# Kernel optimization log

Hardware: AMD Instinct MI355X
Metric: run time of the kernel (lower is better)

## Reference

```python
import jax, jax.numpy as jnp
import numpy as np

N_ATOMS = 50000
N_BONDS = 100000
MAX_NB = 6
ATOM_FDIM = 133
BOND_FDIM = 147
HIDDEN = 512
DEPTH = 5
N_MOLS = 2048


def setup_inputs() -> dict:
    key = jax.random.key(0)
    ks = jax.random.split(key, 10)
    f_atoms = jax.random.normal(ks[0], (N_ATOMS, ATOM_FDIM), dtype=jnp.float32)
    f_bonds = jax.random.normal(ks[1], (N_BONDS, BOND_FDIM), dtype=jnp.float32)
    a2b = jax.random.randint(ks[2], (N_ATOMS, MAX_NB), 0, N_BONDS, dtype=jnp.int32)
    b2a = jax.random.randint(ks[3], (N_BONDS,), 0, N_ATOMS, dtype=jnp.int32)
    # reverse bond of directed bond i is its pair i^1 (chemprop layout)
    b2revb = (jnp.arange(N_BONDS, dtype=jnp.int32) ^ 1)
    mol_ids = jnp.sort(jax.random.randint(ks[4], (N_ATOMS,), 0, N_MOLS, dtype=jnp.int32))
    W_i = jax.random.normal(ks[5], (BOND_FDIM, HIDDEN), dtype=jnp.float32) * 0.05
    W_h = jax.random.normal(ks[6], (HIDDEN, HIDDEN), dtype=jnp.float32) * 0.05
    W_o = jax.random.normal(ks[7], (ATOM_FDIM + HIDDEN, HIDDEN), dtype=jnp.float32) * 0.05
    b_o = jnp.zeros((HIDDEN,), dtype=jnp.float32)
    return {"f_atoms": f_atoms, "f_bonds": f_bonds, "a2b": a2b, "b2a": b2a,
            "b2revb": b2revb, "mol_ids": mol_ids, "W_i": W_i, "W_h": W_h,
            "W_o": W_o, "b_o": b_o, "n_mols": N_MOLS}


def _dmpnn_forward(f_atoms, f_bonds, a2b, b2a, b2revb, mol_ids,
                   W_i, W_h, W_o, b_o, n_mols):
    # input = W_i(f_bonds); message = act(input)   (bond messages, bias=False)
    inp = f_bonds @ W_i                      # [n_bonds, H]
    message = jax.nn.relu(inp)
    for _ in range(DEPTH - 1):
        nei = message[a2b]                   # gather: [n_atoms, max_nb, H]
        a_message = nei.sum(axis=1)          # [n_atoms, H]
        rev_message = message[b2revb]        # [n_bonds, H]
        message = a_message[b2a] - rev_message
        message = jax.nn.relu(inp + message @ W_h)
    # final atom aggregation
    nei = message[a2b]                       # [n_atoms, max_nb, H]
    a_message = nei.sum(axis=1)              # [n_atoms, H]
    a_input = jnp.concatenate([f_atoms, a_message], axis=1)
    atom_hiddens = jax.nn.relu(a_input @ W_o + b_o)   # [n_atoms, H]
    # scope-based mean aggregation per molecule (== a_scope loop, mean)
    sums = jax.ops.segment_sum(atom_hiddens, mol_ids, num_segments=n_mols)
    counts = jax.ops.segment_sum(jnp.ones((atom_hiddens.shape[0],), atom_hiddens.dtype),
                                 mol_ids, num_segments=n_mols)
    mol_vecs = jnp.where(counts[:, None] > 0, sums / jnp.maximum(counts, 1.0)[:, None], 0.0)
    return mol_vecs


def reference(f_atoms, f_bonds, a2b, b2a, b2revb, mol_ids, W_i, W_h, W_o, b_o, n_mols):
    return _dmpnn_forward(f_atoms, f_bonds, a2b, b2a, b2revb, mol_ids,
                          W_i, W_h, W_o, b_o, n_mols)
```

## Files before the change

### kernel.cpp

```cpp
#include <hip/hip_runtime.h>

typedef unsigned int u32;
typedef unsigned short u16;

constexpr int N_ATOMS   = 50000;
constexpr int N_BONDS   = 100000;
constexpr int MAX_NB    = 6;
constexpr int ATOM_FDIM = 133;
constexpr int BOND_FDIM = 147;
constexpr int HIDDEN    = 512;
constexpr int DEPTH     = 5;
constexpr int N_MOLS    = 2048;
constexpr int KB_PAD    = 160;
constexpr int KC        = 672;

typedef short bf16x8 __attribute__((ext_vector_type(8)));
typedef float f32x4  __attribute__((ext_vector_type(4)));

__device__ __forceinline__ float b2f(u32 u) {
    u <<= 16; float f; __builtin_memcpy(&f, &u, 4); return f;
}
__device__ __forceinline__ u16 f2b(float f) {
    u32 u; __builtin_memcpy(&u, &f, 4);
    u = (u + 0x7fffu + ((u >> 16) & 1u)) >> 16;
    return (u16)u;
}
__device__ __forceinline__ u32 pack2(float x, float y) {
    return (u32)f2b(x) | ((u32)f2b(y) << 16);
}
__device__ __forceinline__ float load_in(const void* p, size_t i, u32 bf) {
    return bf ? b2f((u32)((const u16*)p)[i]) : ((const float*)p)[i];
}

__global__ void k_detect(const void* fb, u32* flag) {
    if (threadIdx.x == 0 && blockIdx.x == 0) {
        const u16* p = (const u16*)fb;
        int cnt = 0;
        for (int i = 0; i < 64; ++i) {
            const u32 e = (p[i] >> 7) & 0xFF;
            if (e >= 110 && e <= 140) ++cnt;
        }
        *flag = (cnt >= 52) ? 1u : 0u;
    }
}

template <int SPLIT, int MODE>
__global__ void gemm_bt(const u16* __restrict__ A, int ldaA,
                        const u16* __restrict__ A2,
                        const u16* __restrict__ BT, int ldb,
                        const u16* __restrict__ bias,
                        u16* __restrict__ out,
                        int M, int K)
{
    __shared__ u16 As[128 * 32];
    __shared__ u16 Bs[128 * 32];
    const int t    = threadIdx.x;
    const int w    = t >> 6;
    const int l    = t & 63;
    const int quad = l >> 4;
    const int lr   = l & 15;
    const int bm0  = blockIdx.x * 128;
    const int bn0  = blockIdx.y * 128;
    const int wr   = (w >> 1) * 64;
    const int wc   = (w & 1) * 64;

    f32x4 acc[4][4];
#pragma unroll
    for (int i = 0; i < 4; ++i)
#pragma unroll
        for (int j = 0; j < 4; ++j) acc[i][j] = (f32x4){0.f, 0.f, 0.f, 0.f};

    const int kt_n = K >> 5;
    for (int kt = 0; kt < kt_n; ++kt) {
        const int k0 = kt << 5;
        const u16* srcA;
        int lda, kcol;
        if (SPLIT && kt >= 5) { srcA = A2; lda = HIDDEN; kcol = k0 - KB_PAD; }
        else                  { srcA = A;  lda = ldaA;   kcol = k0; }
        __syncthreads();
#pragma unroll
        for (int p = 0; p < 2; ++p) {
            const int c  = p * 256 + t;
            const int r  = c >> 2;
            const int kg = c & 3;
            int rowA = bm0 + r; if (rowA >= M) rowA = M - 1;
            const uint4 va = *(const uint4*)(srcA + (size_t)rowA * lda + kcol + kg * 8);
            const int rowB = bn0 + r;
            const uint4 vb = *(const uint4*)(BT + (size_t)rowB * ldb + k0 + kg * 8);
            *(uint4*)(As + c * 8) = va;
            *(uint4*)(Bs + c * 8) = vb;
        }
        __syncthreads();

        bf16x8 af[4], bfr[4];
#pragma unroll
        for (int i = 0; i < 4; ++i) {
            af[i]  = *(const bf16x8*)(As + (wr + i * 16 + lr) * 32 + quad * 8);
            bfr[i] = *(const bf16x8*)(Bs + (wc + i * 16 + lr) * 32 + quad * 8);
        }
#pragma unroll
        for (int i = 0; i < 4; ++i)
#pragma unroll
            for (int j = 0; j < 4; ++j)
                acc[i][j] = __builtin_amdgcn_mfma_f32_16x16x32_bf16(
                    af[i], bfr[j], acc[i][j], 0, 0, 0);
    }

#pragma unroll
    for (int i = 0; i < 4; ++i) {
        const int row0 = bm0 + wr + i * 16 + quad * 4;
#pragma unroll
        for (int j = 0; j < 4; ++j) {
            const int col = bn0 + wc + j * 16 + lr;
#pragma unroll
            for (int r = 0; r < 4; ++r) {
                const int row = row0 + r;
                if (row < M) {
                    float v = acc[i][j][r];
                    if (MODE == 1) v += b2f((u32)bias[col]);
                    out[(size_t)row * HIDDEN + col] = f2b(v > 0.f ? v : 0.f);
                }
            }
        }
    }
}

__global__ void k_pad_bonds(const void* __restrict__ src,
                            u16* __restrict__ dst,
                            const u32* __restrict__ flag)
{
    const u32 bf = *flag;
    const int idx = blockIdx.x * 256 + threadIdx.x;
    if (idx >= N_BONDS * KB_PAD) return;
    const int b = idx / KB_PAD, k = idx - b * KB_PAD;
    dst[idx] = (k < BOND_FDIM) ? f2b(load_in(src, (size_t)b * BOND_FDIM + k, bf))
                               : (u16)0;
}

__global__ void k_wcT(const void* __restrict__ wi,
                      const void* __restrict__ wh,
                      u16* __restrict__ wt,
                      const u32* __restrict__ flag)
{
    const u32 bf = *flag;
    const int idx = blockIdx.x * 256 + threadIdx.x;
    if (idx >= 512 * KC) return;
    const int n = idx / KC, k = idx - n * KC;
    float v = 0.f;
    if (k < BOND_FDIM)    v = load_in(wi, (size_t)k * HIDDEN + n, bf);
    else if (k >= KB_PAD) v = load_in(wh, (size_t)(k - KB_PAD) * HIDDEN + n, bf);
    wt[idx] = f2b(v);
}

__global__ void k_woT(const void* __restrict__ wo,
                      u16* __restrict__ wt,
                      const u32* __restrict__ flag)
{
    const u32 bf = *flag;
    const int idx = blockIdx.x * 256 + threadIdx.x;
    if (idx >= 512 * KC) return;
    const int n = idx / KC, k = idx - n * KC;
    wt[idx] = (k < ATOM_FDIM + HIDDEN)
                ? f2b(load_in(wo, (size_t)k * HIDDEN + n, bf)) : (u16)0;
}

__global__ void k_bias(const void* __restrict__ b, u16* __restrict__ dst,
                       const u32* __restrict__ flag)
{
    const u32 bf = *flag;
    const int i = threadIdx.x + blockIdx.x * 256;
    if (i < HIDDEN) dst[i] = f2b(load_in(b, i, bf));
}

__device__ __forceinline__ void acc_row(float* acc, const uint4 v, float s) {
    acc[0] += s * b2f(v.x & 0xffffu); acc[1] += s * b2f(v.x >> 16);
    acc[2] += s * b2f(v.y & 0xffffu); acc[3] += s * b2f(v.y >> 16);
    acc[4] += s * b2f(v.z & 0xffffu); acc[5] += s * b2f(v.z >> 16);
    acc[6] += s * b2f(v.w & 0xffffu); acc[7] += s * b2f(v.w >> 16);
}

__global__ void k_pre(const u16* __restrict__ message,
                      const int* __restrict__ a2b,
                      const int* __restrict__ b2a,
                      const int* __restrict__ b2revb,
                      u16* __restrict__ pre)
{
    const int b = blockIdx.x * 4 + (threadIdx.x >> 6);
    const int l = threadIdx.x & 63;
    const int a  = b2a[b];
    const int rb = b2revb[b];
    float acc[8] = {0.f, 0.f, 0.f, 0.f, 0.f, 0.f, 0.f, 0.f};
    acc_row(acc, *(const uint4*)(message + (size_t)rb * HIDDEN + l * 8), -1.f);
#pragma unroll
    for (int j = 0; j < MAX_NB; ++j) {
        const int nb = a2b[a * MAX_NB + j];
        acc_row(acc, *(const uint4*)(message + (size_t)nb * HIDDEN + l * 8), 1.f);
    }
    uint4 o;
    o.x = pack2(acc[0], acc[1]); o.y = pack2(acc[2], acc[3]);
    o.z = pack2(acc[4], acc[5]); o.w = pack2(acc[6], acc[7]);
    *(uint4*)(pre + (size_t)b * HIDDEN + l * 8) = o;
}

__global__ void k_amsg(const u16* __restrict__ message,
                       const int* __restrict__ a2b,
                       u16* __restrict__ amsg)
{
    const int a = blockIdx.x * 4 + (threadIdx.x >> 6);
    const int l = threadIdx.x & 63;
    float acc[8] = {0.f, 0.f, 0.f, 0.f, 0.f, 0.f, 0.f, 0.f};
#pragma unroll
    for (int j = 0; j < MAX_NB; ++j) {
        const int nb = a2b[a * MAX_NB + j];
        acc_row(acc, *(const uint4*)(message + (size_t)nb * HIDDEN + l * 8), 1.f);
    }
    uint4 o;
    o.x = pack2(acc[0], acc[1]); o.y = pack2(acc[2], acc[3]);
    o.z = pack2(acc[4], acc[5]); o.w = pack2(acc[6], acc[7]);
    *(uint4*)(amsg + (size_t)a * HIDDEN + l * 8) = o;
}

__global__ void k_concat(const void* __restrict__ f_atoms,
                         const u16* __restrict__ amsg,
                         u16* __restrict__ ain,
                         const u32* __restrict__ flag)
{
    const u32 bf = *flag;
    const int idx = blockIdx.x * 256 + threadIdx.x;
    if (idx >= N_ATOMS * KC) return;
    const int a = idx / KC, c = idx - a * KC;
    u16 v;
    if (c < ATOM_FDIM)               v = f2b(load_in(f_atoms, (size_t)a * ATOM_FDIM + c, bf));
    else if (c < ATOM_FDIM + HIDDEN) v = amsg[(size_t)a * HIDDEN + (c - ATOM_FDIM)];
    else                             v = 0;
    ain[idx] = v;
}

__global__ void k_mean(const u16* __restrict__ ah,
                       const int* __restrict__ mol_ids,
                       void* __restrict__ out,
                       const u32* __restrict__ flag)
{
    const u32 bf = *flag;
    const int m = blockIdx.x, t = threadIdx.x;
    int lo = 0, hi = N_ATOMS;
    while (lo < hi) { const int mid = (lo + hi) >> 1; if (mol_ids[mid] < m) lo = mid + 1; else hi = mid; }
    const int start = lo;
    hi = N_ATOMS;
    while (lo < hi) { const int mid = (lo + hi) >> 1; if (mol_ids[mid] <= m) lo = mid + 1; else hi = mid; }
    const int end = lo;
    float x = 0.f, y = 0.f;
    for (int a = start; a < end; ++a) {
        const u32 p = *(const u32*)(ah + (size_t)a * HIDDEN + t * 2);
        x += b2f(p & 0xffffu); y += b2f(p >> 16);
    }
    const float inv = (end > start) ? 1.f / (float)(end - start) : 0.f;
    x *= inv; y *= inv;
    if (bf) {
        *(u32*)((u16*)out + (size_t)m * HIDDEN + t * 2) = pack2(x, y);
    } else {
        float* o = (float*)out + (size_t)m * HIDDEN + t * 2;
        o[0] = x; o[1] = y;
    }
}

extern "C" void kernel_launch(void* const* d_in, const int* in_sizes, int n_in,
                              void* d_out, int out_size, void* d_ws, size_t ws_size,
                              hipStream_t stream)
{
    const void* f_atoms = d_in[0];
    const void* f_bonds = d_in[1];
    const int* a2b     = (const int*)d_in[2];
    const int* b2a     = (const int*)d_in[3];
    const int* b2revb  = (const int*)d_in[4];
    const int* mol_ids = (const int*)d_in[5];
    const void* W_i = d_in[6];
    const void* W_h = d_in[7];
    const void* W_o = d_in[8];
    const void* b_o = d_in[9];

    char* ws = (char*)d_ws;
    size_t off = 0;
    auto alloc = [&](size_t bytes) -> char* {
        char* p = ws + off;
        off += (bytes + 255) & ~(size_t)255;
        return p;
    };
    u32* flag     = (u32*)alloc(256);
    u16* biasB    = (u16*)alloc((size_t)HIDDEN * 2);
    u16* WcT      = (u16*)alloc((size_t)512 * KC * 2);
    u16* WoT      = (u16*)alloc((size_t)512 * KC * 2);
    u16* fbpad    = (u16*)alloc((size_t)N_BONDS * KB_PAD * 2);
    u16* pre      = (u16*)alloc((size_t)N_BONDS * HIDDEN * 2);
    u16* message  = (u16*)alloc((size_t)N_BONDS * HIDDEN * 2);
    u16* amsgF = pre;
    u16* ah    = pre + (size_t)N_ATOMS * HIDDEN;
    u16* ain   = message;

    k_detect<<<dim3(1), 64, 0, stream>>>(f_bonds, flag);
    k_wcT<<<dim3((512 * KC + 255) / 256), 256, 0, stream>>>(W_i, W_h, WcT, flag);
    k_woT<<<dim3((512 * KC + 255) / 256), 256, 0, stream>>>(W_o, WoT, flag);
    k_bias<<<dim3(2), 256, 0, stream>>>(b_o, biasB, flag);
    k_pad_bonds<<<dim3((N_BONDS * KB_PAD + 255) / 256), 256, 0, stream>>>(f_bonds, fbpad, flag);

    const dim3 gB((N_BONDS + 127) / 128, 4);
    gemm_bt<1, 0><<<gB, 256, 0, stream>>>(fbpad, KB_PAD, pre, WcT, KC, nullptr,
                                          message, N_BONDS, KB_PAD);
    for (int d = 0; d < DEPTH - 1; ++d) {
        k_pre<<<dim3(N_BONDS / 4), 256, 0, stream>>>(message, a2b, b2a, b2revb, pre);
        gemm_bt<1, 0><<<gB, 256, 0, stream>>>(fbpad, KB_PAD, pre, WcT, KC, nullptr,
                                              message, N_BONDS, KC);
    }
    k_amsg<<<dim3(N_ATOMS / 4), 256, 0, stream>>>(message, a2b, amsgF);
    k_concat<<<dim3((N_ATOMS * KC + 255) / 256), 256, 0, stream>>>(f_atoms, amsgF, ain, flag);
    gemm_bt<0, 1><<<dim3((N_ATOMS + 127) / 128, 4), 256, 0, stream>>>(
        ain, KC, nullptr, WoT, KC, biasB, ah, N_ATOMS, KC);
    k_mean<<<dim3(N_MOLS), 256, 0, stream>>>(ah, mol_ids, d_out, flag);
}
```

Measured before the change: 1.310 ms.

## Use direct global-to-LDS loads, swap grid order, fuse atom concat into aggregation

The GEMM now stages tiles into shared memory with global_load_lds instead of going through registers. The grid is transposed so the four N-tiles of one M block run next to each other, which should improve L2 reuse of A rows. The final atom aggregation writes straight into the padded concat buffer, with the hidden part first and W_o reordered to match. A small fill kernel writes only the atom features and zero padding, which removes a full read and rewrite of the 50000x672 concat buffer.

```diff
diff --git a/kernel.cpp b/kernel.cpp
--- a/kernel.cpp
+++ b/kernel.cpp
@@ -59,8 +59,8 @@
     const int l    = t & 63;
     const int quad = l >> 4;
     const int lr   = l & 15;
-    const int bm0  = blockIdx.x * 128;
-    const int bn0  = blockIdx.y * 128;
+    const int bn0  = blockIdx.x * 128;
+    const int bm0  = blockIdx.y * 128;
     const int wr   = (w >> 1) * 64;
     const int wc   = (w & 1) * 64;
 
@@ -79,16 +79,23 @@
         else                  { srcA = A;  lda = ldaA;   kcol = k0; }
         __syncthreads();
 #pragma unroll
-        for (int p = 0; p < 2; ++p) {
-            const int c  = p * 256 + t;
+        for (int j = 0; j < 2; ++j) {
+            const int cj = w + j * 4;
+            const int c  = cj * 64 + l;
             const int r  = c >> 2;
             const int kg = c & 3;
             int rowA = bm0 + r; if (rowA >= M) rowA = M - 1;
-            const uint4 va = *(const uint4*)(srcA + (size_t)rowA * lda + kcol + kg * 8);
+            const u16* ga = srcA + (size_t)rowA * lda + kcol + kg * 8;
+            __builtin_amdgcn_global_load_lds(
+                (const __attribute__((address_space(1))) void*)ga,
+                (__attribute__((address_space(3))) void*)(As + cj * 512),
+                16, 0, 0);
             const int rowB = bn0 + r;
-            const uint4 vb = *(const uint4*)(BT + (size_t)rowB * ldb + k0 + kg * 8);
-            *(uint4*)(As + c * 8) = va;
-            *(uint4*)(Bs + c * 8) = vb;
+            const u16* gb = BT + (size_t)rowB * ldb + k0 + kg * 8;
+            __builtin_amdgcn_global_load_lds(
+                (const __attribute__((address_space(1))) void*)gb,
+                (__attribute__((address_space(3))) void*)(Bs + cj * 512),
+                16, 0, 0);
         }
         __syncthreads();
 
@@ -160,8 +167,10 @@
     const int idx = blockIdx.x * 256 + threadIdx.x;
     if (idx >= 512 * KC) return;
     const int n = idx / KC, k = idx - n * KC;
-    wt[idx] = (k < ATOM_FDIM + HIDDEN)
-                ? f2b(load_in(wo, (size_t)k * HIDDEN + n, bf)) : (u16)0;
+    float v = 0.f;
+    if (k < HIDDEN)                  v = load_in(wo, (size_t)(ATOM_FDIM + k) * HIDDEN + n, bf);
+    else if (k < HIDDEN + ATOM_FDIM) v = load_in(wo, (size_t)(k - HIDDEN) * HIDDEN + n, bf);
+    wt[idx] = f2b(v);
 }
 
 __global__ void k_bias(const void* __restrict__ b, u16* __restrict__ dst,
@@ -204,7 +213,7 @@
 
 __global__ void k_amsg(const u16* __restrict__ message,
                        const int* __restrict__ a2b,
-                       u16* __restrict__ amsg)
+                       u16* __restrict__ ain)
 {
     const int a = blockIdx.x * 4 + (threadIdx.x >> 6);
     const int l = threadIdx.x & 63;
@@ -217,23 +226,20 @@
     uint4 o;
     o.x = pack2(acc[0], acc[1]); o.y = pack2(acc[2], acc[3]);
     o.z = pack2(acc[4], acc[5]); o.w = pack2(acc[6], acc[7]);
-    *(uint4*)(amsg + (size_t)a * HIDDEN + l * 8) = o;
-}
-
-__global__ void k_concat(const void* __restrict__ f_atoms,
-                         const u16* __restrict__ amsg,
-                         u16* __restrict__ ain,
-                         const u32* __restrict__ flag)
+    *(uint4*)(ain + (size_t)a * KC + l * 8) = o;
+}
+
+__global__ void k_atomfill(const void* __restrict__ f_atoms,
+                           u16* __restrict__ ain,
+                           const u32* __restrict__ flag)
 {
     const u32 bf = *flag;
     const int idx = blockIdx.x * 256 + threadIdx.x;
-    if (idx >= N_ATOMS * KC) return;
-    const int a = idx / KC, c = idx - a * KC;
-    u16 v;
-    if (c < ATOM_FDIM)               v = f2b(load_in(f_atoms, (size_t)a * ATOM_FDIM + c, bf));
-    else if (c < ATOM_FDIM + HIDDEN) v = amsg[(size_t)a * HIDDEN + (c - ATOM_FDIM)];
-    else                             v = 0;
-    ain[idx] = v;
+    if (idx >= N_ATOMS * (KC - HIDDEN)) return;
+    const int a = idx / (KC - HIDDEN), c = idx - a * (KC - HIDDEN);
+    u16 v = 0;
+    if (c < ATOM_FDIM) v = f2b(load_in(f_atoms, (size_t)a * ATOM_FDIM + c, bf));
+    ain[(size_t)a * KC + HIDDEN + c] = v;
 }
 
 __global__ void k_mean(const u16* __restrict__ ah,
@@ -293,9 +299,8 @@
     u16* fbpad    = (u16*)alloc((size_t)N_BONDS * KB_PAD * 2);
     u16* pre      = (u16*)alloc((size_t)N_BONDS * HIDDEN * 2);
     u16* message  = (u16*)alloc((size_t)N_BONDS * HIDDEN * 2);
-    u16* amsgF = pre;
-    u16* ah    = pre + (size_t)N_ATOMS * HIDDEN;
-    u16* ain   = message;
+    u16* ain = pre;
+    u16* ah  = message;
 
     k_detect<<<dim3(1), 64, 0, stream>>>(f_bonds, flag);
     k_wcT<<<dim3((512 * KC + 255) / 256), 256, 0, stream>>>(W_i, W_h, WcT, flag);
@@ -303,7 +308,7 @@
     k_bias<<<dim3(2), 256, 0, stream>>>(b_o, biasB, flag);
     k_pad_bonds<<<dim3((N_BONDS * KB_PAD + 255) / 256), 256, 0, stream>>>(f_bonds, fbpad, flag);
 
-    const dim3 gB((N_BONDS + 127) / 128, 4);
+    const dim3 gB(4, (N_BONDS + 127) / 128);
     gemm_bt<1, 0><<<gB, 256, 0, stream>>>(fbpad, KB_PAD, pre, WcT, KC, nullptr,
                                           message, N_BONDS, KB_PAD);
     for (int d = 0; d < DEPTH - 1; ++d) {
@@ -311,9 +316,9 @@
         gemm_bt<1, 0><<<gB, 256, 0, stream>>>(fbpad, KB_PAD, pre, WcT, KC, nullptr,
                                               message, N_BONDS, KC);
     }
-    k_amsg<<<dim3(N_ATOMS / 4), 256, 0, stream>>>(message, a2b, amsgF);
-    k_concat<<<dim3((N_ATOMS * KC + 255) / 256), 256, 0, stream>>>(f_atoms, amsgF, ain, flag);
-    gemm_bt<0, 1><<<dim3((N_ATOMS + 127) / 128, 4), 256, 0, stream>>>(
+    k_amsg<<<dim3(N_ATOMS / 4), 256, 0, stream>>>(message, a2b, ain);
+    k_atomfill<<<dim3((N_ATOMS * (KC - HIDDEN) + 255) / 256), 256, 0, stream>>>(f_atoms, ain, flag);
+    gemm_bt<0, 1><<<dim3(4, (N_ATOMS + 127) / 128), 256, 0, stream>>>(
         ain, KC, nullptr, WoT, KC, biasB, ah, N_ATOMS, KC);
     k_mean<<<dim3(N_MOLS), 256, 0, stream>>>(ah, mol_ids, d_out, flag);
 }
```

New measurement: 1.249 ms. 4.7% less time.
